# Optimization experiments

Measured on AMD Instinct MI355X. Metric: run time of the kernel, lower is better.

Reference implementation:

```python
import jax, jax.numpy as jnp
import numpy as np

N_C, N_M, E = 200000, 50000, 1000000
D, H, O = 64, 64, 2


def _seg_mean(msgs, idx, n):
    # mean aggregation as in PyG SAGEConv default; nodes with no in-edges get 0
    s = jax.ops.segment_sum(msgs, idx, num_segments=n)
    c = jax.ops.segment_sum(jnp.ones((msgs.shape[0], 1), msgs.dtype), idx, num_segments=n)
    return s / jnp.maximum(c, 1.0)


def _sage(x_src, x_dst, src, dst, n_dst, Wl, Wr, b):
    agg = _seg_mean(x_src[src], dst, n_dst)  # gather + scatter-mean
    return agg @ Wl + x_dst @ Wr + b


def setup_inputs():
    key = jax.random.key(0)
    ks = jax.random.split(key, 20)

    def lin(k, i, o):
        return (jax.random.normal(k, (i, o), jnp.float32) / np.sqrt(i).astype(np.float32))

    d = {}
    d["x_c"] = jax.random.normal(ks[0], (N_C, D), jnp.float32)
    d["x_m"] = jax.random.normal(ks[1], (N_M, D), jnp.float32)
    d["cm_src"] = jax.random.randint(ks[2], (E,), 0, N_C, jnp.int32)
    d["cm_dst"] = jax.random.randint(ks[3], (E,), 0, N_M, jnp.int32)
    d["mc_src"] = jax.random.randint(ks[4], (E,), 0, N_M, jnp.int32)
    d["mc_dst"] = jax.random.randint(ks[5], (E,), 0, N_C, jnp.int32)
    # layer 1 (per edge type: neighbor weight Wl, root weight Wr, bias)
    d["Wl1_cm"] = lin(ks[6], D, H); d["Wr1_cm"] = lin(ks[7], D, H); d["b1_cm"] = jnp.zeros((H,), jnp.float32)
    d["Wl1_mc"] = lin(ks[8], D, H); d["Wr1_mc"] = lin(ks[9], D, H); d["b1_mc"] = jnp.zeros((H,), jnp.float32)
    # layer 2
    d["Wl2_cm"] = lin(ks[10], H, H); d["Wr2_cm"] = lin(ks[11], H, H); d["b2_cm"] = jnp.zeros((H,), jnp.float32)
    d["Wl2_mc"] = lin(ks[12], H, H); d["Wr2_mc"] = lin(ks[13], H, H); d["b2_mc"] = jnp.zeros((H,), jnp.float32)
    # final linear on customer nodes
    d["W_lin"] = lin(ks[14], H, O); d["b_lin"] = jnp.zeros((O,), jnp.float32)
    return d


def reference(x_c, x_m, cm_src, cm_dst, mc_src, mc_dst,
              Wl1_cm, Wr1_cm, b1_cm, Wl1_mc, Wr1_mc, b1_mc,
              Wl2_cm, Wr2_cm, b2_cm, Wl2_mc, Wr2_mc, b2_mc,
              W_lin, b_lin):
    # conv1: hetero SAGE, aggr='sum' across edge types (one per dst type here)
    h_m = _sage(x_c, x_m, cm_src, cm_dst, N_M, Wl1_cm, Wr1_cm, b1_cm)
    h_c = _sage(x_m, x_c, mc_src, mc_dst, N_C, Wl1_mc, Wr1_mc, b1_mc)
    h_m = jax.nn.relu(h_m)
    h_c = jax.nn.relu(h_c)
    # conv2
    h2_m = _sage(h_c, h_m, cm_src, cm_dst, N_M, Wl2_cm, Wr2_cm, b2_cm)
    h2_c = _sage(h_m, h_c, mc_src, mc_dst, N_C, Wl2_mc, Wr2_mc, b2_mc)
    # final linear on customer nodes (h2_m unused, as in original module)
    del h2_m
    return h2_c @ W_lin + b_lin
```

## Files before the change

### kernel.cpp

```cpp
#include <hip/hip_runtime.h>

#define NC 200000
#define NM 50000
#define NE 1000000
#define DF 64

#define BSH_M 8
#define BW_M 256
#define NBM ((NM + BW_M - 1) >> BSH_M)
#define BSH_C 10
#define BW_C 1024
#define NBC ((NC + BW_C - 1) >> BSH_C)
#define CH 4096
#define NSB ((NE + CH - 1) / CH)
#define PSB 1024

typedef __attribute__((ext_vector_type(8))) short bf16x8;
typedef __attribute__((ext_vector_type(4))) float f32x4;
typedef __attribute__((ext_vector_type(4))) unsigned short u16x4;

__device__ __forceinline__ short bf16rn(float x) {
    unsigned u = __builtin_bit_cast(unsigned, x);
    unsigned r = u + 0x7FFFu + ((u >> 16) & 1u);
    return (short)(r >> 16);
}
__device__ __forceinline__ float bf16f(short h) {
    unsigned u = ((unsigned)(unsigned short)h) << 16;
    return __builtin_bit_cast(float, u);
}
__device__ __forceinline__ void split8(const f32x4 u, const f32x4 v,
                                       bf16x8& hi, bf16x8& lo) {
#pragma unroll
    for (int b = 0; b < 4; ++b) {
        short h = bf16rn(u[b]);
        hi[b] = h;
        lo[b] = bf16rn(u[b] - bf16f(h));
    }
#pragma unroll
    for (int b = 0; b < 4; ++b) {
        short h = bf16rn(v[b]);
        hi[4 + b] = h;
        lo[4 + b] = bf16rn(v[b] - bf16f(h));
    }
}

__device__ __forceinline__ int wscan_incl(int v, int lane) {
#pragma unroll
    for (int off = 1; off < 64; off <<= 1) {
        int y = __shfl_up(v, off);
        if (lane >= off) v += y;
    }
    return v;
}

__global__ __launch_bounds__(256) void prep_k(const int* __restrict__ cm_dst,
                                              const int* __restrict__ mc_dst,
                                              int* __restrict__ pmM,
                                              int* __restrict__ pmC,
                                              const float* __restrict__ x_c,
                                              const float* __restrict__ x_m,
                                              u16x4* __restrict__ xc16,
                                              u16x4* __restrict__ xm16,
                                              const float* __restrict__ Wl2,
                                              const float* __restrict__ Wr2,
                                              const float* __restrict__ b2,
                                              const float* __restrict__ Wlin,
                                              const float* __restrict__ blin,
                                              float* __restrict__ Vl,
                                              float* __restrict__ Vr,
                                              float* __restrict__ bo) {
    __shared__ int cnt[256];
    const int t = threadIdx.x;
    if (blockIdx.x < 2 * NSB) {
        const int side = (blockIdx.x >= NSB);
        const int blk = blockIdx.x - side * NSB;
        const int* dst = side ? mc_dst : cm_dst;
        int* pm = side ? pmC : pmM;
        const int nb = side ? NBC : NBM;
        const int bsh = side ? BSH_C : BSH_M;
        cnt[t] = 0;
        __syncthreads();
        const int e0 = blk * CH;
        const int n = min(CH, NE - e0);
        for (int i = t; i < n; i += 256) atomicAdd(&cnt[dst[e0 + i] >> bsh], 1);
        __syncthreads();
        if (t < nb) pm[(long)blk * nb + t] = cnt[t];
    } else if (blockIdx.x < 2 * NSB + PSB) {
        const int blk = blockIdx.x - 2 * NSB;
        const int NC4 = NC * (DF / 4);
        const int NT4 = (NC + NM) * (DF / 4);
        const int st = PSB * 256;
        for (int i = blk * 256 + t; i < NT4; i += st) {
            const bool isc = (i < NC4);
            const int j = isc ? i : i - NC4;
            const f32x4 v = isc ? ((const f32x4*)x_c)[j] : ((const f32x4*)x_m)[j];
            u16x4 o;
#pragma unroll
            for (int b = 0; b < 4; ++b) o[b] = (unsigned short)bf16rn(v[b]);
            if (isc) xc16[j] = o;
            else     xm16[j] = o;
        }
    } else {
        for (int i = t; i < 2 * 64 * 16; i += 256) {
            float* dst = (i < 1024) ? Vl : Vr;
            dst[i & 1023] = 0.0f;
        }
        __syncthreads();
        if (t < 128) {
            const int k = t >> 1, o = t & 1;
            float sl = 0.f, sr = 0.f;
            for (int j = 0; j < 64; ++j) {
                sl += Wl2[k * 64 + j] * Wlin[j * 2 + o];
                sr += Wr2[k * 64 + j] * Wlin[j * 2 + o];
            }
            Vl[k * 16 + o] = sl;
            Vr[k * 16 + o] = sr;
        }
        if (t < 2) {
            float s = blin[t];
            for (int j = 0; j < 64; ++j) s += b2[j] * Wlin[j * 2 + t];
            bo[t] = s;
        }
    }
}

__global__ __launch_bounds__(256) void cred2_k(const int* __restrict__ pmM,
                                               const int* __restrict__ pmC,
                                               int* __restrict__ totM,
                                               int* __restrict__ totC) {
    __shared__ int red[256];
    const int side = (blockIdx.x >= NBM);
    const int b = blockIdx.x - side * NBM;
    const int* pm = side ? pmC : pmM;
    const int nb = side ? NBC : NBM;
    int* tot = side ? totC : totM;
    const int t = threadIdx.x;
    int s = 0;
    for (int i = t; i < NSB; i += 256) s += pm[(long)i * nb + b];
    red[t] = s;
    __syncthreads();
    for (int off = 128; off > 0; off >>= 1) {
        if (t < off) red[t] += red[t + off];
        __syncthreads();
    }
    if (t == 0) tot[b] = red[0];
}

__global__ __launch_bounds__(256) void cscan3_k(const int* __restrict__ totM,
                                                const int* __restrict__ totC,
                                                int* __restrict__ cstartM,
                                                int* __restrict__ cstartC,
                                                int* __restrict__ ccurM,
                                                int* __restrict__ ccurC) {
    __shared__ int wsum[4];
    const int t = threadIdx.x, lane = t & 63, wv = t >> 6;
    int s = (t < NBM) ? totM[t] : 0;
    int incl = wscan_incl(s, lane);
    if (lane == 63) wsum[wv] = incl;
    __syncthreads();
    int wadd = 0;
#pragma unroll
    for (int w = 0; w < 4; ++w) wadd += (w < wv) ? wsum[w] : 0;
    const int tot = incl + wadd;
    if (t < NBM) { cstartM[t] = tot - s; ccurM[t] = tot - s; }
    if (t == NBM - 1) cstartM[NBM] = tot;
    __syncthreads();
    int s2 = (t < NBC) ? totC[t] : 0;
    int incl2 = wscan_incl(s2, lane);
    if (lane == 63) wsum[wv] = incl2;
    __syncthreads();
    int wadd2 = 0;
#pragma unroll
    for (int w = 0; w < 4; ++w) wadd2 += (w < wv) ? wsum[w] : 0;
    const int tot2 = incl2 + wadd2;
    if (t < NBC) { cstartC[t] = tot2 - s2; ccurC[t] = tot2 - s2; }
    if (t == NBC - 1) cstartC[NBC] = tot2;
}

__global__ __launch_bounds__(256) void bsort2_k(const int* __restrict__ cm_src,
                                                const int* __restrict__ cm_dst,
                                                const int* __restrict__ mc_src,
                                                const int* __restrict__ mc_dst,
                                                int* __restrict__ ccurM,
                                                int* __restrict__ ccurC,
                                                int* __restrict__ bktM,
                                                int* __restrict__ bktC) {
    __shared__ int cnt[256], pfx[256], gbase[256];
    __shared__ int wsum[4];
    __shared__ int stage[CH];
    const int side = (blockIdx.x >= NSB);
    const int blk = blockIdx.x - side * NSB;
    const int* src = side ? mc_src : cm_src;
    const int* dst = side ? mc_dst : cm_dst;
    int* ccur = side ? ccurC : ccurM;
    int* bkt = side ? bktC : bktM;
    const int nb = side ? NBC : NBM;
    const int bsh = side ? BSH_C : BSH_M;
    const int bmask = (side ? BW_C : BW_M) - 1;

    const int t = threadIdx.x, lane = t & 63, wv = t >> 6;
    const int e0 = blk * CH;
    const int n = min(CH, NE - e0);
    cnt[t] = 0;
    __syncthreads();
    for (int i = t; i < n; i += 256) atomicAdd(&cnt[dst[e0 + i] >> bsh], 1);
    __syncthreads();
    const int myc = (t < nb) ? cnt[t] : 0;
    int incl = wscan_incl(myc, lane);
    if (lane == 63) wsum[wv] = incl;
    __syncthreads();
    int wadd = 0;
#pragma unroll
    for (int w = 0; w < 4; ++w) wadd += (w < wv) ? wsum[w] : 0;
    const int excl = wadd + incl - myc;
    if (t < nb && myc > 0) gbase[t] = atomicAdd(&ccur[t], myc);
    pfx[t] = excl;
    cnt[t] = 0;
    __syncthreads();
    for (int i = t; i < n; i += 256) {
        const int d = dst[e0 + i];
        const int b = d >> bsh;
        const int p = pfx[b] + atomicAdd(&cnt[b], 1);
        stage[p] = (src[e0 + i] << bsh) | (d & bmask);
    }
    __syncthreads();
    for (int b = wv; b < nb; b += 4) {
        const int c = cnt[b];
        if (c == 0) continue;
        const int gb = gbase[b], lo = pfx[b];
        for (int j = lane; j < c; j += 64) bkt[gb + j] = stage[lo + j];
    }
}

__global__ __launch_bounds__(256) void bp22_k(const int* __restrict__ bktM,
                                              const int* __restrict__ cstartM,
                                              int* __restrict__ startM,
                                              int* __restrict__ srtM,
                                              const int* __restrict__ bktC,
                                              const int* __restrict__ cstartC,
                                              int* __restrict__ startC,
                                              int* __restrict__ srtC) {
    __shared__ int lcur[BW_C];
    __shared__ int wsum[4];
    const int side = (blockIdx.x >= NBM);
    const int blk = blockIdx.x - side * NBM;
    const int* bkt = side ? bktC : bktM;
    const int* cstart = side ? cstartC : cstartM;
    int* start = side ? startC : startM;
    int* srt = side ? srtC : srtM;
    const int n_nodes = side ? NC : NM;
    const int bw = side ? BW_C : BW_M;
    const int bsh = side ? BSH_C : BSH_M;
    const int base = blk << bsh;
    const int t = threadIdx.x, lane = t & 63, wv = t >> 6;

    const int e0 = cstart[blk];
    const int e1 = cstart[blk + 1];

    for (int i = t; i < bw; i += 256) lcur[i] = 0;
    __syncthreads();
    for (int e = e0 + t; e < e1; e += 256) atomicAdd(&lcur[bkt[e] & (bw - 1)], 1);
    __syncthreads();

    int c0 = 0, c1 = 0, c2 = 0, c3 = 0;
    const bool act = (4 * t < bw);
    if (act) {
        c0 = lcur[4 * t + 0]; c1 = lcur[4 * t + 1];
        c2 = lcur[4 * t + 2]; c3 = lcur[4 * t + 3];
    }
    const int local = c0 + c1 + c2 + c3;
    int incl = wscan_incl(local, lane);
    if (lane == 63) wsum[wv] = incl;
    __syncthreads();
    int wadd = 0;
#pragma unroll
    for (int w = 0; w < 4; ++w) wadd += (w < wv) ? wsum[w] : 0;
    const int p0 = e0 + wadd + incl - local;
    const int p1 = p0 + c0, p2 = p1 + c1, p3 = p2 + c2;
    if (act) {
        lcur[4 * t + 0] = p0;
        lcur[4 * t + 1] = p1;
        lcur[4 * t + 2] = p2;
        lcur[4 * t + 3] = p3;
        if (base + 4 * t + 0 < n_nodes) start[base + 4 * t + 0] = p0;
        if (base + 4 * t + 1 < n_nodes) start[base + 4 * t + 1] = p1;
        if (base + 4 * t + 2 < n_nodes) start[base + 4 * t + 2] = p2;
        if (base + 4 * t + 3 < n_nodes) start[base + 4 * t + 3] = p3;
    }
    if (t == 0 && base + bw >= n_nodes) start[n_nodes] = e1;
    __syncthreads();

    for (int e = e0 + t; e < e1; e += 256) {
        const int p = bkt[e];
        const int pos = atomicAdd(&lcur[p & (bw - 1)], 1);
        srt[pos] = p >> bsh;
    }
}

__global__ __launch_bounds__(256) void agg16_k(const unsigned short* __restrict__ xhi,
                                               const int* __restrict__ start,
                                               const int* __restrict__ srt,
                                               unsigned short* __restrict__ mean16,
                                               int n_nodes) {
    const int sgid = (blockIdx.x * blockDim.x + threadIdx.x) >> 4;
    const int nsg = (gridDim.x * blockDim.x) >> 4;
    const int k4 = (threadIdx.x & 15) * 4;
    for (int n = sgid; n < n_nodes; n += nsg) {
        const int s0 = start[n], s1 = start[n + 1];
        f32x4 a0 = {0.f, 0.f, 0.f, 0.f}, a1 = {0.f, 0.f, 0.f, 0.f};
        f32x4 a2 = {0.f, 0.f, 0.f, 0.f}, a3 = {0.f, 0.f, 0.f, 0.f};
        int e = s0;
        for (; e + 3 < s1; e += 4) {
            const int i0 = srt[e + 0], i1 = srt[e + 1];
            const int i2 = srt[e + 2], i3 = srt[e + 3];
            const u16x4 v0 = *(const u16x4*)(xhi + (long)i0 * DF + k4);
            const u16x4 v1 = *(const u16x4*)(xhi + (long)i1 * DF + k4);
            const u16x4 v2 = *(const u16x4*)(xhi + (long)i2 * DF + k4);
            const u16x4 v3 = *(const u16x4*)(xhi + (long)i3 * DF + k4);
#pragma unroll
            for (int c = 0; c < 4; ++c) {
                a0[c] += bf16f((short)v0[c]);
                a1[c] += bf16f((short)v1[c]);
                a2[c] += bf16f((short)v2[c]);
                a3[c] += bf16f((short)v3[c]);
            }
        }
        for (; e < s1; ++e) {
            const int i0 = srt[e];
            const u16x4 v0 = *(const u16x4*)(xhi + (long)i0 * DF + k4);
#pragma unroll
            for (int c = 0; c < 4; ++c) a0[c] += bf16f((short)v0[c]);
        }
        const float inv = 1.0f / fmaxf((float)(s1 - s0), 1.0f);
        u16x4 o;
#pragma unroll
        for (int c = 0; c < 4; ++c)
            o[c] = (unsigned short)bf16rn(((a0[c] + a1[c]) + (a2[c] + a3[c])) * inv);
        *(u16x4*)(mean16 + (long)n * DF + k4) = o;
    }
}

__global__ __launch_bounds__(256) void aggc2_k(const unsigned short* __restrict__ xp,
                                               const float* __restrict__ zm,
                                               const int* __restrict__ start,
                                               const int* __restrict__ srt,
                                               unsigned short* __restrict__ mx,
                                               float* __restrict__ mz, int n_nodes) {
    const int sgid = (blockIdx.x * blockDim.x + threadIdx.x) >> 4;
    const int nsg = (gridDim.x * blockDim.x) >> 4;
    const int k4 = (threadIdx.x & 15) * 4;
    for (int n = sgid; n < n_nodes; n += nsg) {
        const int s0 = start[n], s1 = start[n + 1];
        f32x4 ax0 = {0.f, 0.f, 0.f, 0.f}, ax1 = {0.f, 0.f, 0.f, 0.f};
        float z0 = 0.f, z1 = 0.f;
        int e = s0;
        for (; e + 1 < s1; e += 2) {
            const int iA = srt[e], iB = srt[e + 1];
            const u16x4 vxA = *(const u16x4*)(xp + (long)iA * DF + k4);
            const u16x4 vxB = *(const u16x4*)(xp + (long)iB * DF + k4);
            const float2 zA = *(const float2*)(zm + (long)iA * 2);
            const float2 zB = *(const float2*)(zm + (long)iB * 2);
#pragma unroll
            for (int c = 0; c < 4; ++c) {
                ax0[c] += bf16f((short)vxA[c]);
                ax1[c] += bf16f((short)vxB[c]);
            }
            z0 += zA.x + zB.x;
            z1 += zA.y + zB.y;
        }
        if (e < s1) {
            const int iA = srt[e];
            const u16x4 vxA = *(const u16x4*)(xp + (long)iA * DF + k4);
            const float2 zA = *(const float2*)(zm + (long)iA * 2);
#pragma unroll
            for (int c = 0; c < 4; ++c) ax0[c] += bf16f((short)vxA[c]);
            z0 += zA.x;
            z1 += zA.y;
        }
        const float inv = 1.0f / fmaxf((float)(s1 - s0), 1.0f);
        u16x4 ox;
#pragma unroll
        for (int c = 0; c < 4; ++c)
            ox[c] = (unsigned short)bf16rn((ax0[c] + ax1[c]) * inv);
        *(u16x4*)(mx + (long)n * DF + k4) = ox;
        if ((threadIdx.x & 15) == 0) {
            mz[(long)n * 2 + 0] = z0 * inv;
            mz[(long)n * 2 + 1] = z1 * inv;
        }
    }
}

#define MFMA(a, b, c) __builtin_amdgcn_mfma_f32_16x16x32_bf16((a), (b), (c), 0, 0, 0)

#define LOAD_W(Wl, Wr, col, g, wlh, wll, wrh, wrl)          \
    do {                                                    \
        _Pragma("unroll")                                   \
        for (int q = 0; q < 2; ++q) {                       \
            f32x4 tl0, tl1, tr0, tr1;                       \
            _Pragma("unroll")                               \
            for (int b = 0; b < 4; ++b) {                   \
                int k = 32 * q + 8 * (g) + b;               \
                tl0[b] = (Wl)[k * DF + (col)];              \
                tr0[b] = (Wr)[k * DF + (col)];              \
                tl1[b] = (Wl)[(k + 4) * DF + (col)];        \
                tr1[b] = (Wr)[(k + 4) * DF + (col)];        \
            }                                               \
            split8(tl0, tl1, wlh[q], wll[q]);               \
            split8(tr0, tr1, wrh[q], wrl[q]);               \
        }                                                   \
    } while (0)

#define LOAD_V(V, col, g, vh, vlo)                          \
    do {                                                    \
        _Pragma("unroll")                                   \
        for (int q = 0; q < 2; ++q) {                       \
            f32x4 t0, t1;                                   \
            _Pragma("unroll")                               \
            for (int b = 0; b < 4; ++b) {                   \
                int k = 32 * q + 8 * (g) + b;               \
                t0[b] = (V)[k * 16 + (col)];                \
                t1[b] = (V)[(k + 4) * 16 + (col)];          \
            }                                               \
            split8(t0, t1, vh[q], vlo[q]);                  \
        }                                                   \
    } while (0)

__global__ __launch_bounds__(256) void dense1nm_k(const unsigned short* __restrict__ mean16,
                                                  const unsigned short* __restrict__ xm16,
                                                  const float* __restrict__ Wl,
                                                  const float* __restrict__ Wr,
                                                  const float* __restrict__ bias,
                                                  const float* __restrict__ Vl,
                                                  float* __restrict__ zm,
                                                  int n_nodes) {
    __shared__ float sZ[2][4][16][2];
    const int t = threadIdx.x;
    const int lane = t & 63;
    const int wv = t >> 6;
    const int col = wv * 16 + (lane & 15);
    const int g = lane >> 4;

    bf16x8 wlh[2], wll[2], wrh[2], wrl[2];
    LOAD_W(Wl, Wr, col, g, wlh, wll, wrh, wrl);
    const float bv = bias[col];
    const float vl0 = Vl[col * 16 + 0];
    const float vl1 = Vl[col * 16 + 1];

    const int nrt = n_nodes >> 4;
    int par = 0;
    for (int rt = blockIdx.x; rt < nrt; rt += gridDim.x, par ^= 1) {
        const long rowA = (long)rt * 16 + (lane & 15);
        const bf16x8 m0 = *(const bf16x8*)(mean16 + rowA * DF + 8 * g);
        const bf16x8 m1 = *(const bf16x8*)(mean16 + rowA * DF + 32 + 8 * g);
        const bf16x8 x0 = *(const bf16x8*)(xm16 + rowA * DF + 8 * g);
        const bf16x8 x1 = *(const bf16x8*)(xm16 + rowA * DF + 32 + 8 * g);
        f32x4 acc = {0.f, 0.f, 0.f, 0.f};
        acc = MFMA(m0, wlh[0], acc);
        acc = MFMA(m0, wll[0], acc);
        acc = MFMA(m1, wlh[1], acc);
        acc = MFMA(m1, wll[1], acc);
        acc = MFMA(x0, wrh[0], acc);
        acc = MFMA(x0, wrl[0], acc);
        acc = MFMA(x1, wrh[1], acc);
        acc = MFMA(x1, wrl[1], acc);

        float z0[4], z1[4];
#pragma unroll
        for (int r = 0; r < 4; ++r) {
            const float h = fmaxf(acc[r] + bv, 0.0f);
            z0[r] = h * vl0;
            z1[r] = h * vl1;
        }
#pragma unroll
        for (int m = 1; m < 16; m <<= 1) {
#pragma unroll
            for (int r = 0; r < 4; ++r) {
                z0[r] += __shfl_xor(z0[r], m);
                z1[r] += __shfl_xor(z1[r], m);
            }
        }
        if ((lane & 15) == 0) {
#pragma unroll
            for (int r = 0; r < 4; ++r) {
                sZ[par][wv][4 * g + r][0] = z0[r];
                sZ[par][wv][4 * g + r][1] = z1[r];
            }
        }
        __syncthreads();
        if (t < 16) {
            const long node = (long)rt * 16 + t;
            const float a = sZ[par][0][t][0] + sZ[par][1][t][0] +
                            sZ[par][2][t][0] + sZ[par][3][t][0];
            const float b = sZ[par][0][t][1] + sZ[par][1][t][1] +
                            sZ[par][2][t][1] + sZ[par][3][t][1];
            zm[node * 2 + 0] = a;
            zm[node * 2 + 1] = b;
        }
    }
}

__global__ __launch_bounds__(256) void densec_k(const unsigned short* __restrict__ meanx,
                                                const float* __restrict__ meanz,
                                                const unsigned short* __restrict__ xc,
                                                const float* __restrict__ Wl1,
                                                const float* __restrict__ Wr1,
                                                const float* __restrict__ b1,
                                                const float* __restrict__ Vr,
                                                const float* __restrict__ bo,
                                                float* __restrict__ out, int n_nodes) {
    __shared__ unsigned short sH[2][16][72];
    const int t = threadIdx.x;
    const int lane = t & 63;
    const int wv = t >> 6;
    const int col = wv * 16 + (lane & 15);
    const int g = lane >> 4;

    bf16x8 w1lh[2], w1ll[2], w1rh[2], w1rl[2];
    LOAD_W(Wl1, Wr1, col, g, w1lh, w1ll, w1rh, w1rl);
    const float bv1 = b1[col];
    bf16x8 vrh[2], vrl[2];
    LOAD_V(Vr, (lane & 15), g, vrh, vrl);
    const int oc = lane & 15;
    const float bo2 = (oc < 2) ? bo[oc] : 0.0f;

    const int nrt = n_nodes >> 4;
    int par = 0;
    for (int rt = blockIdx.x; rt < nrt; rt += gridDim.x, par ^= 1) {
        const long rowA = (long)rt * 16 + (lane & 15);
        const bf16x8 mx0 = *(const bf16x8*)(meanx + rowA * DF + 8 * g);
        const bf16x8 mx1 = *(const bf16x8*)(meanx + rowA * DF + 32 + 8 * g);
        const bf16x8 xc0 = *(const bf16x8*)(xc + rowA * DF + 8 * g);
        const bf16x8 xc1 = *(const bf16x8*)(xc + rowA * DF + 32 + 8 * g);
        float mzv[4];
        if (oc < 2) {
#pragma unroll
            for (int r = 0; r < 4; ++r)
                mzv[r] = meanz[((long)rt * 16 + 4 * g + r) * 2 + oc];
        }

        f32x4 acc = {0.f, 0.f, 0.f, 0.f};
        acc = MFMA(mx0, w1lh[0], acc);
        acc = MFMA(mx0, w1ll[0], acc);
        acc = MFMA(mx1, w1lh[1], acc);
        acc = MFMA(mx1, w1ll[1], acc);
        acc = MFMA(xc0, w1rh[0], acc);
        acc = MFMA(xc0, w1rl[0], acc);
        acc = MFMA(xc1, w1rh[1], acc);
        acc = MFMA(xc1, w1rl[1], acc);
#pragma unroll
        for (int r = 0; r < 4; ++r)
            sH[par][4 * g + r][col] = (unsigned short)bf16rn(fmaxf(acc[r] + bv1, 0.0f));
        __syncthreads();

        const bf16x8 hc0 = *(const bf16x8*)&sH[par][lane & 15][8 * g];
        const bf16x8 hc1 = *(const bf16x8*)&sH[par][lane & 15][32 + 8 * g];
        f32x4 a2 = {0.f, 0.f, 0.f, 0.f};
        a2 = MFMA(hc0, vrh[0], a2);
        a2 = MFMA(hc0, vrl[0], a2);
        a2 = MFMA(hc1, vrh[1], a2);
        a2 = MFMA(hc1, vrl[1], a2);
        if (oc < 2) {
#pragma unroll
            for (int r = 0; r < 4; ++r) {
                const long node = (long)rt * 16 + 4 * g + r;
                out[node * 2 + oc] = a2[r] + mzv[r] + bo2;
            }
        }
    }
}

extern "C" void kernel_launch(void* const* d_in, const int* in_sizes, int n_in,
                              void* d_out, int out_size, void* d_ws, size_t ws_size,
                              hipStream_t stream) {
    const float* x_c = (const float*)d_in[0];
    const float* x_m = (const float*)d_in[1];
    const int* cm_src = (const int*)d_in[2];
    const int* cm_dst = (const int*)d_in[3];
    const int* mc_src = (const int*)d_in[4];
    const int* mc_dst = (const int*)d_in[5];
    const float* Wl1_cm = (const float*)d_in[6];
    const float* Wr1_cm = (const float*)d_in[7];
    const float* b1_cm = (const float*)d_in[8];
    const float* Wl1_mc = (const float*)d_in[9];
    const float* Wr1_mc = (const float*)d_in[10];
    const float* b1_mc = (const float*)d_in[11];
    const float* Wl2_mc = (const float*)d_in[15];
    const float* Wr2_mc = (const float*)d_in[16];
    const float* b2_mc = (const float*)d_in[17];
    const float* W_lin = (const float*)d_in[18];
    const float* b_lin = (const float*)d_in[19];
    float* out = (float*)d_out;

    unsigned short* up = (unsigned short*)d_ws;
    unsigned short* aggm16 = up;
    unsigned short* xm16 = aggm16 + (long)NM * DF;
    unsigned short* xc16 = xm16 + (long)NM * DF;
    unsigned short* meanx16 = xc16 + (long)NC * DF;
    float* zm = (float*)(meanx16 + (long)NC * DF);
    float* meanz = zm + (long)NM * 2;
    float* Vl = meanz + (long)NC * 2;
    float* Vr = Vl + 64 * 16;
    float* bo = Vr + 64 * 16;
    int* ip = (int*)(bo + 4);

    int* startM = ip;
    int* startC = startM + (NM + 1);
    int* cstartM = startC + (NC + 1);
    int* cstartC = cstartM + (NBM + 1);
    int* ccurM = cstartC + (NBC + 1);
    int* ccurC = ccurM + NBM;
    int* totM = ccurC + NBC;
    int* totC = totM + NBM;
    int* pmM = totC + NBC;
    int* pmC = pmM + NSB * NBM;
    int* srt_cm = pmC + NSB * NBC;
    int* srt_mc = srt_cm + NE;
    int* bktM = srt_mc + NE;
    int* bktC = bktM + NE;

    prep_k<<<2 * NSB + PSB + 1, 256, 0, stream>>>(cm_dst, mc_dst, pmM, pmC,
                                                  x_c, x_m, (u16x4*)xc16, (u16x4*)xm16,
                                                  Wl2_mc, Wr2_mc, b2_mc, W_lin, b_lin,
                                                  Vl, Vr, bo);
    cred2_k<<<NBM + NBC, 256, 0, stream>>>(pmM, pmC, totM, totC);
    cscan3_k<<<1, 256, 0, stream>>>(totM, totC, cstartM, cstartC, ccurM, ccurC);
    bsort2_k<<<2 * NSB, 256, 0, stream>>>(cm_src, cm_dst, mc_src, mc_dst,
                                          ccurM, ccurC, bktM, bktC);
    bp22_k<<<NBM + NBC, 256, 0, stream>>>(bktM, cstartM, startM, srt_cm,
                                          bktC, cstartC, startC, srt_mc);

    agg16_k<<<NM / 16, 256, 0, stream>>>(xc16, startM, srt_cm, aggm16, NM);
    dense1nm_k<<<1024, 256, 0, stream>>>(aggm16, xm16, Wl1_cm, Wr1_cm, b1_cm,
                                         Vl, zm, NM);

    aggc2_k<<<NC / 16, 256, 0, stream>>>(xm16, zm, startC, srt_mc,
                                         meanx16, meanz, NC);

    densec_k<<<2048, 256, 0, stream>>>(meanx16, meanz, xc16,
                                       Wl1_mc, Wr1_mc, b1_mc,
                                       Vr, bo, out, NC);
}
```

Measured before the change: 176.3 us.

## Reuse precomputed bucket counts in sort and merge both feature aggregations

The bucket-sort kernel now reads the per-chunk bucket histograms already produced by the prep kernel instead of recounting destinations with shared atomics. Both 64-wide bf16 mean aggregations (customer→merchant and merchant→customer) now run in one launch. The small 2-wide z aggregation that depends on the dense1 output is split into its own lightweight kernel with one thread per node. This removes a redundant pass over dst and a serial dependency between the large customer aggregation and dense1, at the cost of an extra pass over the CSR indices for z.

```diff
diff --git a/kernel.cpp b/kernel.cpp
--- a/kernel.cpp
+++ b/kernel.cpp
@@ -181,6 +181,8 @@
                                                 const int* __restrict__ cm_dst,
                                                 const int* __restrict__ mc_src,
                                                 const int* __restrict__ mc_dst,
+                                                const int* __restrict__ pmM,
+                                                const int* __restrict__ pmC,
                                                 int* __restrict__ ccurM,
                                                 int* __restrict__ ccurC,
                                                 int* __restrict__ bktM,
@@ -192,6 +194,7 @@
     const int blk = blockIdx.x - side * NSB;
     const int* src = side ? mc_src : cm_src;
     const int* dst = side ? mc_dst : cm_dst;
+    const int* pm = side ? pmC : pmM;
     int* ccur = side ? ccurC : ccurM;
     int* bkt = side ? bktC : bktM;
     const int nb = side ? NBC : NBM;
@@ -201,11 +204,7 @@
     const int t = threadIdx.x, lane = t & 63, wv = t >> 6;
     const int e0 = blk * CH;
     const int n = min(CH, NE - e0);
-    cnt[t] = 0;
-    __syncthreads();
-    for (int i = t; i < n; i += 256) atomicAdd(&cnt[dst[e0 + i] >> bsh], 1);
-    __syncthreads();
-    const int myc = (t < nb) ? cnt[t] : 0;
+    const int myc = (t < nb) ? pm[(long)blk * nb + t] : 0;
     int incl = wscan_incl(myc, lane);
     if (lane == 63) wsum[wv] = incl;
     __syncthreads();
@@ -297,96 +296,87 @@
     }
 }
 
-__global__ __launch_bounds__(256) void agg16_k(const unsigned short* __restrict__ xhi,
-                                               const int* __restrict__ start,
-                                               const int* __restrict__ srt,
-                                               unsigned short* __restrict__ mean16,
-                                               int n_nodes) {
-    const int sgid = (blockIdx.x * blockDim.x + threadIdx.x) >> 4;
-    const int nsg = (gridDim.x * blockDim.x) >> 4;
-    const int k4 = (threadIdx.x & 15) * 4;
-    for (int n = sgid; n < n_nodes; n += nsg) {
+__device__ __forceinline__ void agg_node16(const unsigned short* __restrict__ xhi,
+                                           const int* __restrict__ start,
+                                           const int* __restrict__ srt,
+                                           unsigned short* __restrict__ mean16,
+                                           int n, int k4) {
+    const int s0 = start[n], s1 = start[n + 1];
+    f32x4 a0 = {0.f, 0.f, 0.f, 0.f}, a1 = {0.f, 0.f, 0.f, 0.f};
+    f32x4 a2 = {0.f, 0.f, 0.f, 0.f}, a3 = {0.f, 0.f, 0.f, 0.f};
+    int e = s0;
+    for (; e + 3 < s1; e += 4) {
+        const int i0 = srt[e + 0], i1 = srt[e + 1];
+        const int i2 = srt[e + 2], i3 = srt[e + 3];
+        const u16x4 v0 = *(const u16x4*)(xhi + (long)i0 * DF + k4);
+        const u16x4 v1 = *(const u16x4*)(xhi + (long)i1 * DF + k4);
+        const u16x4 v2 = *(const u16x4*)(xhi + (long)i2 * DF + k4);
+        const u16x4 v3 = *(const u16x4*)(xhi + (long)i3 * DF + k4);
+#pragma unroll
+        for (int c = 0; c < 4; ++c) {
+            a0[c] += bf16f((short)v0[c]);
+            a1[c] += bf16f((short)v1[c]);
+            a2[c] += bf16f((short)v2[c]);
+            a3[c] += bf16f((short)v3[c]);
+        }
+    }
+    for (; e < s1; ++e) {
+        const int i0 = srt[e];
+        const u16x4 v0 = *(const u16x4*)(xhi + (long)i0 * DF + k4);
+#pragma unroll
+        for (int c = 0; c < 4; ++c) a0[c] += bf16f((short)v0[c]);
+    }
+    const float inv = 1.0f / fmaxf((float)(s1 - s0), 1.0f);
+    u16x4 o;
+#pragma unroll
+    for (int c = 0; c < 4; ++c)
+        o[c] = (unsigned short)bf16rn(((a0[c] + a1[c]) + (a2[c] + a3[c])) * inv);
+    *(u16x4*)(mean16 + (long)n * DF + k4) = o;
+}
+
+__global__ __launch_bounds__(256) void aggall_k(const unsigned short* __restrict__ xc16,
+                                                const int* __restrict__ startM,
+                                                const int* __restrict__ srt_cm,
+                                                unsigned short* __restrict__ aggm16,
+                                                const unsigned short* __restrict__ xm16,
+                                                const int* __restrict__ startC,
+                                                const int* __restrict__ srt_mc,
+                                                unsigned short* __restrict__ meanx16) {
+    const int t = threadIdx.x;
+    const int sg = t >> 4;
+    const int k4 = (t & 15) * 4;
+    if (blockIdx.x < NM / 16) {
+        const int n = blockIdx.x * 16 + sg;
+        agg_node16(xc16, startM, srt_cm, aggm16, n, k4);
+    } else {
+        const int n = (blockIdx.x - NM / 16) * 16 + sg;
+        agg_node16(xm16, startC, srt_mc, meanx16, n, k4);
+    }
+}
+
+__global__ __launch_bounds__(256) void aggz_k(const float2* __restrict__ zm,
+                                              const int* __restrict__ start,
+                                              const int* __restrict__ srt,
+                                              float2* __restrict__ meanz, int n_nodes) {
+    int n = blockIdx.x * blockDim.x + threadIdx.x;
+    const int st = gridDim.x * blockDim.x;
+    for (; n < n_nodes; n += st) {
         const int s0 = start[n], s1 = start[n + 1];
-        f32x4 a0 = {0.f, 0.f, 0.f, 0.f}, a1 = {0.f, 0.f, 0.f, 0.f};
-        f32x4 a2 = {0.f, 0.f, 0.f, 0.f}, a3 = {0.f, 0.f, 0.f, 0.f};
-        int e = s0;
-        for (; e + 3 < s1; e += 4) {
-            const int i0 = srt[e + 0], i1 = srt[e + 1];
-            const int i2 = srt[e + 2], i3 = srt[e + 3];
-            const u16x4 v0 = *(const u16x4*)(xhi + (long)i0 * DF + k4);
-            const u16x4 v1 = *(const u16x4*)(xhi + (long)i1 * DF + k4);
-            const u16x4 v2 = *(const u16x4*)(xhi + (long)i2 * DF + k4);
-            const u16x4 v3 = *(const u16x4*)(xhi + (long)i3 * DF + k4);
-#pragma unroll
-            for (int c = 0; c < 4; ++c) {
-                a0[c] += bf16f((short)v0[c]);
-                a1[c] += bf16f((short)v1[c]);
-                a2[c] += bf16f((short)v2[c]);
-                a3[c] += bf16f((short)v3[c]);
-            }
-        }
-        for (; e < s1; ++e) {
-            const int i0 = srt[e];
-            const u16x4 v0 = *(const u16x4*)(xhi + (long)i0 * DF + k4);
-#pragma unroll
-            for (int c = 0; c < 4; ++c) a0[c] += bf16f((short)v0[c]);
-        }
-        const float inv = 1.0f / fmaxf((float)(s1 - s0), 1.0f);
-        u16x4 o;
-#pragma unroll
-        for (int c = 0; c < 4; ++c)
-            o[c] = (unsigned short)bf16rn(((a0[c] + a1[c]) + (a2[c] + a3[c])) * inv);
-        *(u16x4*)(mean16 + (long)n * DF + k4) = o;
-    }
-}
-
-__global__ __launch_bounds__(256) void aggc2_k(const unsigned short* __restrict__ xp,
-                                               const float* __restrict__ zm,
-                                               const int* __restrict__ start,
-                                               const int* __restrict__ srt,
-                                               unsigned short* __restrict__ mx,
-                                               float* __restrict__ mz, int n_nodes) {
-    const int sgid = (blockIdx.x * blockDim.x + threadIdx.x) >> 4;
-    const int nsg = (gridDim.x * blockDim.x) >> 4;
-    const int k4 = (threadIdx.x & 15) * 4;
-    for (int n = sgid; n < n_nodes; n += nsg) {
-        const int s0 = start[n], s1 = start[n + 1];
-        f32x4 ax0 = {0.f, 0.f, 0.f, 0.f}, ax1 = {0.f, 0.f, 0.f, 0.f};
-        float z0 = 0.f, z1 = 0.f;
+        float z0 = 0.f, z1 = 0.f, y0 = 0.f, y1 = 0.f;
         int e = s0;
         for (; e + 1 < s1; e += 2) {
-            const int iA = srt[e], iB = srt[e + 1];
-            const u16x4 vxA = *(const u16x4*)(xp + (long)iA * DF + k4);
-            const u16x4 vxB = *(const u16x4*)(xp + (long)iB * DF + k4);
-            const float2 zA = *(const float2*)(zm + (long)iA * 2);
-            const float2 zB = *(const float2*)(zm + (long)iB * 2);
-#pragma unroll
-            for (int c = 0; c < 4; ++c) {
-                ax0[c] += bf16f((short)vxA[c]);
-                ax1[c] += bf16f((short)vxB[c]);
-            }
-            z0 += zA.x + zB.x;
-            z1 += zA.y + zB.y;
+            const float2 a = zm[srt[e]];
+            const float2 b = zm[srt[e + 1]];
+            z0 += a.x; z1 += a.y;
+            y0 += b.x; y1 += b.y;
         }
         if (e < s1) {
-            const int iA = srt[e];
-            const u16x4 vxA = *(const u16x4*)(xp + (long)iA * DF + k4);
-            const float2 zA = *(const float2*)(zm + (long)iA * 2);
-#pragma unroll
-            for (int c = 0; c < 4; ++c) ax0[c] += bf16f((short)vxA[c]);
-            z0 += zA.x;
-            z1 += zA.y;
+            const float2 a = zm[srt[e]];
+            z0 += a.x; z1 += a.y;
         }
         const float inv = 1.0f / fmaxf((float)(s1 - s0), 1.0f);
-        u16x4 ox;
-#pragma unroll
-        for (int c = 0; c < 4; ++c)
-            ox[c] = (unsigned short)bf16rn((ax0[c] + ax1[c]) * inv);
-        *(u16x4*)(mx + (long)n * DF + k4) = ox;
-        if ((threadIdx.x & 15) == 0) {
-            mz[(long)n * 2 + 0] = z0 * inv;
-            mz[(long)n * 2 + 1] = z1 * inv;
-        }
+        float2 o = {(z0 + y0) * inv, (z1 + y1) * inv};
+        meanz[n] = o;
     }
 }
 
@@ -625,16 +615,18 @@
     cred2_k<<<NBM + NBC, 256, 0, stream>>>(pmM, pmC, totM, totC);
     cscan3_k<<<1, 256, 0, stream>>>(totM, totC, cstartM, cstartC, ccurM, ccurC);
     bsort2_k<<<2 * NSB, 256, 0, stream>>>(cm_src, cm_dst, mc_src, mc_dst,
-                                          ccurM, ccurC, bktM, bktC);
+                                          pmM, pmC, ccurM, ccurC, bktM, bktC);
     bp22_k<<<NBM + NBC, 256, 0, stream>>>(bktM, cstartM, startM, srt_cm,
                                           bktC, cstartC, startC, srt_mc);
 
-    agg16_k<<<NM / 16, 256, 0, stream>>>(xc16, startM, srt_cm, aggm16, NM);
+    aggall_k<<<NM / 16 + NC / 16, 256, 0, stream>>>(xc16, startM, srt_cm, aggm16,
+                                                    xm16, startC, srt_mc, meanx16);
+
     dense1nm_k<<<1024, 256, 0, stream>>>(aggm16, xm16, Wl1_cm, Wr1_cm, b1_cm,
                                          Vl, zm, NM);
 
-    aggc2_k<<<NC / 16, 256, 0, stream>>>(xm16, zm, startC, srt_mc,
-                                         meanx16, meanz, NC);
+    aggz_k<<<782, 256, 0, stream>>>((const float2*)zm, startC, srt_mc,
+                                    (float2*)meanz, NC);
 
     densec_k<<<2048, 256, 0, stream>>>(meanx16, meanz, xc16,
                                        Wl1_mc, Wr1_mc, b1_mc,
```

Measured after the change: 170.2 us (median of 2 runs). -3.4%, faster.
